# Performance work log

Measured on AMD Instinct MI355X. Metric: run time of the kernel, lower is better.

## Reference

```python
import jax, jax.numpy as jnp
import numpy as np

LN_EPS = 1e-5

def _layernorm(x, g, b):
    mu = jnp.mean(x, axis=-1, keepdims=True)
    var = jnp.mean(jnp.square(x - mu), axis=-1, keepdims=True)
    return (x - mu) * jax.lax.rsqrt(var + LN_EPS) * g + b

def setup_inputs() -> dict:
    key = jax.random.key(0)
    ks = jax.random.split(key, 8)
    B, T, C = 4, 2048, 1024
    s = 0.02
    return {
        "x": jax.random.normal(ks[0], (B, T, C), jnp.float32),
        "w_qkv": jax.random.normal(ks[1], (C, 3 * C), jnp.float32) * s,
        "b_qkv": jnp.zeros((3 * C,), jnp.float32),
        "w_out": jax.random.normal(ks[2], (C, C), jnp.float32) * s,
        "b_out": jnp.zeros((C,), jnp.float32),
        "w1": jax.random.normal(ks[3], (C, 4 * C), jnp.float32) * s,
        "b1": jnp.zeros((4 * C,), jnp.float32),
        "w2": jax.random.normal(ks[4], (4 * C, C), jnp.float32) * s,
        "b2": jnp.zeros((C,), jnp.float32),
        "g1": jnp.ones((C,), jnp.float32),
        "be1": jnp.zeros((C,), jnp.float32),
        "g2": jnp.ones((C,), jnp.float32),
        "be2": jnp.zeros((C,), jnp.float32),
        "n_head": 16,
    }

def reference(x, w_qkv, b_qkv, w_out, b_out, w1, b1, w2, b2, g1, be1, g2, be2, n_head):
    B, T, C = x.shape
    H = n_head
    D = C // H
    # --- causal self-attention ---
    qkv = x @ w_qkv + b_qkv                      # [B,T,3C]
    q, k, v = jnp.split(qkv, 3, axis=-1)
    q = q.reshape(B, T, H, D).transpose(0, 2, 1, 3)  # [B,H,T,D]
    k = k.reshape(B, T, H, D).transpose(0, 2, 1, 3)
    v = v.reshape(B, T, H, D).transpose(0, 2, 1, 3)
    attn = jnp.einsum("bhqd,bhkd->bhqk", q, k) * (1.0 / np.sqrt(D))
    causal = jnp.tril(jnp.ones((T, T), bool))
    attn = jnp.where(causal, attn, jnp.float32(-jnp.inf))
    attn = jax.nn.softmax(attn, axis=-1)
    y = jnp.einsum("bhqk,bhkd->bhqd", attn, v)
    y = y.transpose(0, 2, 1, 3).reshape(B, T, C)
    y = y @ w_out + b_out
    # post-norm residual (norm applied to sublayer output)
    x = x + _layernorm(y, g1, be1)
    # --- MLP ---
    h = jax.nn.gelu(x @ w1 + b1, approximate=False)
    h = h @ w2 + b2
    x = x + _layernorm(h, g2, be2)
    return x
```

## Files before the change

kernel.cpp:

```cpp
#include <hip/hip_runtime.h>
#include <hip/hip_bf16.h>

typedef unsigned short ushort_t;
using bf16x8 = __attribute__((ext_vector_type(8))) short;
using f32x4  = __attribute__((ext_vector_type(4))) float;

#define DEV __device__ __forceinline__

DEV unsigned short f2bf(float f) {
    unsigned int u = __builtin_bit_cast(unsigned int, f);
    u = (u + 0x7fffu + ((u >> 16) & 1u)) >> 16;
    return (unsigned short)u;
}

DEV int cvtpk_bf16(float lo, float hi) {
    int r;
    asm("v_cvt_pk_bf16_f32 %0, %1, %2" : "=v"(r) : "v"(lo), "v"(hi));
    return r;
}

DEV void gload16(const unsigned short* g, unsigned short* l) {
    __builtin_amdgcn_global_load_lds(
        (const __attribute__((address_space(1))) void*)g,
        (__attribute__((address_space(3))) void*)l, 16, 0, 0);
}

DEV float gelu_f(float v) {
    float u = v * (0.79788456f + 0.03567741f * v * v);
    float t = __builtin_amdgcn_exp2f(u * 2.88539008f);
    return v * t * __builtin_amdgcn_rcpf(t + 1.0f);
}

__global__ __launch_bounds__(256) void cvtbf_kernel(const float* __restrict__ in,
                                                    unsigned short* __restrict__ out) {
    int i = (blockIdx.x * 256 + threadIdx.x) * 4;
    float4 v = *(const float4*)&in[i];
    out[i + 0] = f2bf(v.x);
    out[i + 1] = f2bf(v.y);
    out[i + 2] = f2bf(v.z);
    out[i + 3] = f2bf(v.w);
}

__global__ __launch_bounds__(256) void transpose_cvt_kernel(const float* __restrict__ in,
                                                            unsigned short* __restrict__ out,
                                                            int R, int C) {
    __shared__ float t[32][33];
    int tx = threadIdx.x, ty = threadIdx.y;
    int c0 = blockIdx.x * 32, r0 = blockIdx.y * 32;
#pragma unroll
    for (int i = 0; i < 4; ++i)
        t[ty + i * 8][tx] = in[(size_t)(r0 + ty + i * 8) * C + c0 + tx];
    __syncthreads();
#pragma unroll
    for (int i = 0; i < 4; ++i)
        out[(size_t)(c0 + ty + i * 8) * R + r0 + tx] = f2bf(t[tx][ty + i * 8]);
}

__global__ __launch_bounds__(256) void vtrans_kernel(const unsigned short* __restrict__ qkvb,
                                                     unsigned short* __restrict__ vtg) {
    __shared__ unsigned short t[64 * 66];
    const int tid = threadIdx.x;
    const int t0 = blockIdx.x * 64;
    const int bh = blockIdx.y;
    const int b = bh >> 4, h = bh & 15;
    const unsigned short* src = qkvb + (size_t)(b * 2048 + t0) * 3072 + 2048 + h * 64;
#pragma unroll
    for (int c = 0; c < 2; ++c) {
        int cid = c * 256 + tid;
        int row = cid >> 3, cc = cid & 7;
        *(int4*)&t[row * 66 + cc * 8] = *(const int4*)&src[(size_t)row * 3072 + cc * 8];
    }
    __syncthreads();
    unsigned short* dst = vtg + (size_t)bh * 64 * 2048 + t0;
#pragma unroll
    for (int c = 0; c < 2; ++c) {
        int cid = c * 256 + tid;
        int d = cid >> 3, cc2 = cid & 7;
        bf16x8 v;
#pragma unroll
        for (int j = 0; j < 8; ++j) v[j] = (short)t[(cc2 * 8 + j) * 66 + d];
        *(bf16x8*)&dst[(size_t)d * 2048 + cc2 * 8] = v;
    }
}

template <int BM, int ACT, int OBF>
__global__ __launch_bounds__(512, 2) void gemm256_kernel(
    const unsigned short* __restrict__ A, const unsigned short* __restrict__ Bt,
    const float* __restrict__ bias, void* __restrict__ out,
    int N, int K, int gridNt) {
    constexpr int MF = BM / 32;
    constexpr int ALD = BM / 64;
    constexpr int NW = ALD / 2 + 2;
    constexpr int LB = (BM == 256) ? 8 : 7;
    __shared__ __align__(16) unsigned short lA[2][BM * 64];
    __shared__ __align__(16) unsigned short lB[2][256 * 64];
    const int tid = threadIdx.x;
    const int lane = tid & 63, wid = tid >> 6;
    const int g = lane >> 4, lr = lane & 15;
    const int wm = wid >> 2, wn = wid & 3;

    const int nwg = gridDim.x, cpx = nwg >> 3, bid = blockIdx.x;
    const int wkid = (bid & 7) * cpx + (bid >> 3);
    const int mt = wkid / gridNt, nt = wkid % gridNt;
    const int m0 = mt * BM, n0 = nt * 256;

    auto stageA = [&](int s, int kt, int bb) {
        int c = s * 512 + tid;
        int row = c & (BM - 1), kb = c >> LB;
        gload16(&A[(size_t)(m0 + row) * K + kt * 64 + kb * 8],
                &lA[bb][(size_t)(s * 512 + (tid & ~63)) * 8]);
    };
    auto stageB = [&](int s, int kt, int bb) {
        int c = s * 512 + tid;
        int row = c & 255, kb = c >> 8;
        gload16(&Bt[(size_t)(n0 + row) * K + kt * 64 + kb * 8],
                &lB[bb][(size_t)(s * 512 + (tid & ~63)) * 8]);
    };
    auto stageKh = [&](int half, int kt, int bb) {
        if constexpr (BM == 256) {
            stageA(half * 2 + 0, kt, bb);
            stageA(half * 2 + 1, kt, bb);
            stageB(half * 2 + 0, kt, bb);
            stageB(half * 2 + 1, kt, bb);
        } else {
            stageA(half, kt, bb);
            stageB(half * 2 + 0, kt, bb);
            stageB(half * 2 + 1, kt, bb);
        }
    };

    f32x4 acc[MF][4] = {};
    bf16x8 af[MF];
    bf16x8 bfr[4];

    const int nkt = K >> 6;
    stageKh(0, 0, 0);
    stageKh(1, 0, 0);

    for (int kt = 0; kt < nkt; ++kt) {
        const int b = kt & 1;
        const bool more = (kt + 1 < nkt);
#pragma unroll
        for (int ks = 0; ks < 2; ++ks) {
            if (ks == 1 && !more)
                asm volatile("s_waitcnt vmcnt(0)" ::: "memory");
            else if constexpr (BM == 256)
                asm volatile("s_waitcnt vmcnt(4)" ::: "memory");
            else
                asm volatile("s_waitcnt vmcnt(3)" ::: "memory");
            __builtin_amdgcn_s_barrier();
            asm volatile("" ::: "memory");
#pragma unroll
            for (int mf = 0; mf < MF; ++mf) {
                int c = (ks * 4 + g) * BM + wm * (BM / 2) + mf * 16 + lr;
                af[mf] = *(const bf16x8*)&lA[b][(size_t)c * 8];
            }
#pragma unroll
            for (int nf = 0; nf < 4; ++nf) {
                int c = (ks * 4 + g) * 256 + wn * 64 + nf * 16 + lr;
                bfr[nf] = *(const bf16x8*)&lB[b][(size_t)c * 8];
            }
            if (more) stageKh(ks, kt + 1, b ^ 1);
            __builtin_amdgcn_s_setprio(1);
#pragma unroll
            for (int mf = 0; mf < MF; ++mf)
#pragma unroll
                for (int nf = 0; nf < 4; ++nf)
                    acc[mf][nf] = __builtin_amdgcn_mfma_f32_16x16x32_bf16(
                        af[mf], bfr[nf], acc[mf][nf], 0, 0, 0);
            __builtin_amdgcn_s_setprio(0);
        }
    }

#pragma unroll
    for (int mf = 0; mf < MF; ++mf) {
#pragma unroll
        for (int nf = 0; nf < 4; ++nf) {
            int col = n0 + wn * 64 + nf * 16 + lr;
            float bv = bias[col];
#pragma unroll
            for (int r = 0; r < 4; ++r) {
                int row = m0 + wm * (BM / 2) + mf * 16 + g * 4 + r;
                float v = acc[mf][nf][r] + bv;
                if (ACT == 1) v = gelu_f(v);
                if (OBF)
                    ((unsigned short*)out)[(size_t)row * N + col] = f2bf(v);
                else
                    ((float*)out)[(size_t)row * N + col] = v;
            }
        }
    }
}

__global__ __launch_bounds__(256) void attn_kernel(const unsigned short* __restrict__ qkv,
                                                   const unsigned short* __restrict__ vtg,
                                                   unsigned short* __restrict__ y) {
    __shared__ unsigned short Kl[2][4096];
    __shared__ unsigned short Vl[2][4096];
    const int tid = threadIdx.x, lane = tid & 63, w = tid >> 6;
    const int g = lane >> 4, lr = lane & 15;
    const int p = blockIdx.x, h = blockIdx.y, b = blockIdx.z;
    const int bh = b * 16 + h;
    const size_t rs3 = 3072;
    const unsigned short* qbase = qkv + (size_t)b * 2048 * rs3 + h * 64;
    const unsigned short* kbase = qbase + 1024;
    const unsigned short* vbase = vtg + (size_t)bh * 64 * 2048;

    int ksoff[2], vsoff[2], ldoff[2];
#pragma unroll
    for (int c = 0; c < 2; ++c) {
        int row = w * 16 + c * 8 + (lane >> 3);
        int ccs = (lane & 7) ^ (row & 7) ^ (row >> 3);
        ksoff[c] = row * 3072 + ccs * 8;
        vsoff[c] = row * 2048 + ccs * 8;
        ldoff[c] = (w * 16 + c * 8) * 64;
    }

    const int idxP0 = 4 * (32 * (g & 1) + lr);
    const int idxP1 = idxP0 + 64;
    int idxA[4];
#pragma unroll
    for (int r = 0; r < 4; ++r) idxA[r] = 4 * (g * 20 + r);
    const bool ghigh = (g >> 1) != 0;
    const float qscale = 0.125f * 1.44269504089f;

    auto process = [&](int J) {
        const int q0w = J * 128 + w * 32;
        const int ktend = 2 * J + 2;
#pragma unroll
        for (int c = 0; c < 2; ++c) {
            gload16(&kbase[ksoff[c]], &Kl[0][ldoff[c]]);
            gload16(&vbase[vsoff[c]], &Vl[0][ldoff[c]]);
        }
        int qf[2][2][4];
#pragma unroll
        for (int sub = 0; sub < 2; ++sub)
#pragma unroll
            for (int f = 0; f < 2; ++f) {
                int4 v = *(const int4*)&qbase[(size_t)(q0w + sub * 16 + lr) * rs3 + f * 32 + g * 8];
                int vv[4] = {v.x, v.y, v.z, v.w};
#pragma unroll
                for (int i = 0; i < 4; ++i) {
                    unsigned int u = (unsigned int)vv[i];
                    float lo = __builtin_bit_cast(float, u << 16) * qscale;
                    float hi = __builtin_bit_cast(float, u & 0xffff0000u) * qscale;
                    qf[sub][f][i] = cvtpk_bf16(lo, hi);
                }
            }

        f32x4 O[2][4] = {};
        float m_[2] = {-3.0e38f, -3.0e38f}, l_[2] = {0.f, 0.f};

        int buf = 0;
        for (int kt = 0; kt < ktend; ++kt) {
            asm volatile("s_waitcnt vmcnt(0)" ::: "memory");
            __builtin_amdgcn_s_barrier();
            asm volatile("" ::: "memory");
            if (kt + 1 < ktend) {
#pragma unroll
                for (int c = 0; c < 2; ++c) {
                    gload16(&kbase[(size_t)(kt + 1) * 64 * 3072 + ksoff[c]], &Kl[buf ^ 1][ldoff[c]]);
                    gload16(&vbase[vsoff[c] + (kt + 1) * 64], &Vl[buf ^ 1][ldoff[c]]);
                }
            }
            const unsigned short* Kc = Kl[buf];
            const unsigned short* Vc = Vl[buf];

            const bool act0 = (kt * 64) <= (q0w + 15);
            const bool act1 = (kt * 64) <= (q0w + 31);

            f32x4 s0[4], s1[4];
#pragma unroll
            for (int st = 0; st < 4; ++st) {
                int rbase = (st * 16 + lr) * 64;
                int sw = (lr & 7) ^ (st * 2 + (lr >> 3));
                bf16x8 kf0 = *(const bf16x8*)&Kc[rbase + ((g ^ sw) * 8)];
                bf16x8 kf1 = *(const bf16x8*)&Kc[rbase + (((4 + g) ^ sw) * 8)];
                if (act0) {
                    f32x4 a = {};
                    a = __builtin_amdgcn_mfma_f32_16x16x32_bf16(kf0, *(const bf16x8*)&qf[0][0], a, 0, 0, 0);
                    a = __builtin_amdgcn_mfma_f32_16x16x32_bf16(kf1, *(const bf16x8*)&qf[0][1], a, 0, 0, 0);
                    s0[st] = a;
                }
                if (act1) {
                    f32x4 a = {};
                    a = __builtin_amdgcn_mfma_f32_16x16x32_bf16(kf0, *(const bf16x8*)&qf[1][0], a, 0, 0, 0);
                    a = __builtin_amdgcn_mfma_f32_16x16x32_bf16(kf1, *(const bf16x8*)&qf[1][1], a, 0, 0, 0);
                    s1[st] = a;
                }
            }

            int wt0[2][4], wt1[2][4];
#pragma unroll
            for (int sub = 0; sub < 2; ++sub) {
                if (sub == 0 && !act0) continue;
                if (sub == 1 && !act1) continue;
                f32x4* s = (sub == 0) ? s0 : s1;
                const int qmin = q0w + sub * 16;
                if (kt * 64 + 63 > qmin) {
                    int qv = qmin + lr;
#pragma unroll
                    for (int st = 0; st < 4; ++st) {
                        int keyb = kt * 64 + st * 16 + g * 4;
#pragma unroll
                        for (int r = 0; r < 4; ++r)
                            if (keyb + r > qv) s[st][r] = -3.0e38f;
                    }
                }
                float mx = fmaxf(fmaxf(s[0][0], s[0][1]), fmaxf(s[0][2], s[0][3]));
#pragma unroll
                for (int st = 1; st < 4; ++st)
                    mx = fmaxf(mx, fmaxf(fmaxf(s[st][0], s[st][1]), fmaxf(s[st][2], s[st][3])));
                mx = fmaxf(mx, __shfl_xor(mx, 16));
                mx = fmaxf(mx, __shfl_xor(mx, 32));
                float mold = m_[sub];
                float mnew = fmaxf(mold, mx);
                float alpha = __builtin_amdgcn_exp2f(mold - mnew);
                m_[sub] = mnew;
                float rs = 0.f;
#pragma unroll
                for (int st = 0; st < 4; ++st)
#pragma unroll
                    for (int r = 0; r < 4; ++r) {
                        float pp = __builtin_amdgcn_exp2f(s[st][r] - mnew);
                        s[st][r] = pp;
                        rs += pp;
                    }
                rs += __shfl_xor(rs, 16);
                rs += __shfl_xor(rs, 32);
                l_[sub] = l_[sub] * alpha + rs;
                int av = __builtin_bit_cast(int, alpha);
                f32x4* Os = O[sub];
#pragma unroll
                for (int r = 0; r < 4; ++r) {
                    float ar = __builtin_bit_cast(float, __builtin_amdgcn_ds_bpermute(idxA[r], av));
#pragma unroll
                    for (int dt = 0; dt < 4; ++dt) Os[dt][r] *= ar;
                }
                int ws_[4][2];
#pragma unroll
                for (int st = 0; st < 4; ++st) {
                    ws_[st][0] = cvtpk_bf16(s[st][0], s[st][1]);
                    ws_[st][1] = cvtpk_bf16(s[st][2], s[st][3]);
                }
                int(*wt)[4] = (sub == 0) ? wt0 : wt1;
#pragma unroll
                for (int ks = 0; ks < 2; ++ks)
#pragma unroll
                    for (int hp = 0; hp < 4; ++hp) {
                        int idx = (hp < 2) ? idxP0 : idxP1;
                        int v0 = __builtin_amdgcn_ds_bpermute(idx, ws_[2 * ks][hp & 1]);
                        int v1 = __builtin_amdgcn_ds_bpermute(idx, ws_[2 * ks + 1][hp & 1]);
                        wt[ks][hp] = ghigh ? v1 : v0;
                    }
            }

#pragma unroll
            for (int ks = 0; ks < 2; ++ks) {
                bf16x8 pa0 = *(const bf16x8*)&wt0[ks][0];
                bf16x8 pa1 = *(const bf16x8*)&wt1[ks][0];
#pragma unroll
                for (int dt = 0; dt < 4; ++dt) {
                    int d = dt * 16 + lr;
                    int xv = (ks * 4 + g) ^ (lr & 7) ^ (dt * 2 + (lr >> 3));
                    bf16x8 vf = *(const bf16x8*)&Vc[d * 64 + xv * 8];
                    if (act0) O[0][dt] = __builtin_amdgcn_mfma_f32_16x16x32_bf16(pa0, vf, O[0][dt], 0, 0, 0);
                    if (act1) O[1][dt] = __builtin_amdgcn_mfma_f32_16x16x32_bf16(pa1, vf, O[1][dt], 0, 0, 0);
                }
            }
            buf ^= 1;
        }

#pragma unroll
        for (int sub = 0; sub < 2; ++sub) {
            int lv = __builtin_bit_cast(int, l_[sub]);
#pragma unroll
            for (int r = 0; r < 4; ++r) {
                float lval = __builtin_bit_cast(float, __builtin_amdgcn_ds_bpermute(idxA[r], lv));
                float inv = __builtin_amdgcn_rcpf(lval);
                int q = q0w + sub * 16 + g * 4 + r;
#pragma unroll
                for (int dt = 0; dt < 4; ++dt)
                    y[(size_t)(b * 2048 + q) * 1024 + h * 64 + dt * 16 + lr] =
                        f2bf(O[sub][dt][r] * inv);
            }
        }
    };

    process(15 - p);
    __syncthreads();
    process(p);
}

template <int WRITE_BF>
__global__ __launch_bounds__(256) void ln_kernel(const float* __restrict__ base,
                                                 const float* __restrict__ delta,
                                                 const float* __restrict__ gw,
                                                 const float* __restrict__ bw,
                                                 float* __restrict__ outf,
                                                 unsigned short* __restrict__ outb) {
    const int row = blockIdx.x;
    const int tid = threadIdx.x;
    const float* d = delta + (size_t)row * 1024;
    const float* bs = base + (size_t)row * 1024;
    float4 x = *(const float4*)&d[tid * 4];
    float s = x.x + x.y + x.z + x.w;
    float s2 = x.x * x.x + x.y * x.y + x.z * x.z + x.w * x.w;
#pragma unroll
    for (int off = 1; off < 64; off <<= 1) {
        s += __shfl_xor(s, off);
        s2 += __shfl_xor(s2, off);
    }
    __shared__ float red[8];
    if ((tid & 63) == 0) {
        red[tid >> 6] = s;
        red[4 + (tid >> 6)] = s2;
    }
    __syncthreads();
    s = red[0] + red[1] + red[2] + red[3];
    s2 = red[4] + red[5] + red[6] + red[7];
    float mu = s * (1.f / 1024.f);
    float var = s2 * (1.f / 1024.f) - mu * mu;
    float rsig = rsqrtf(var + 1e-5f);
    float4 bb = *(const float4*)&bs[tid * 4];
    float4 gv = *(const float4*)&gw[tid * 4];
    float4 bv = *(const float4*)&bw[tid * 4];
    float4 o;
    o.x = bb.x + (x.x - mu) * rsig * gv.x + bv.x;
    o.y = bb.y + (x.y - mu) * rsig * gv.y + bv.y;
    o.z = bb.z + (x.z - mu) * rsig * gv.z + bv.z;
    o.w = bb.w + (x.w - mu) * rsig * gv.w + bv.w;
    *(float4*)&outf[(size_t)row * 1024 + tid * 4] = o;
    if (WRITE_BF) {
        unsigned short* ob = outb + (size_t)row * 1024 + tid * 4;
        ob[0] = f2bf(o.x);
        ob[1] = f2bf(o.y);
        ob[2] = f2bf(o.z);
        ob[3] = f2bf(o.w);
    }
}

extern "C" void kernel_launch(void* const* d_in, const int* in_sizes, int n_in,
                              void* d_out, int out_size, void* d_ws, size_t ws_size,
                              hipStream_t stream) {
    const float* x = (const float*)d_in[0];
    const float* w_qkv = (const float*)d_in[1];
    const float* b_qkv = (const float*)d_in[2];
    const float* w_out = (const float*)d_in[3];
    const float* b_out = (const float*)d_in[4];
    const float* w1 = (const float*)d_in[5];
    const float* b1 = (const float*)d_in[6];
    const float* w2 = (const float*)d_in[7];
    const float* b2 = (const float*)d_in[8];
    const float* g1 = (const float*)d_in[9];
    const float* be1 = (const float*)d_in[10];
    const float* g2 = (const float*)d_in[11];
    const float* be2 = (const float*)d_in[12];

    const size_t MB = 1ull << 20;
    if (ws_size < 184 * MB) return;
    char* ws = (char*)d_ws;
    unsigned short* xb    = (unsigned short*)(ws + 0);
    unsigned short* vtg   = (unsigned short*)(ws + 0);
    unsigned short* wqkvt = (unsigned short*)(ws + 16 * MB);
    unsigned short* qkvb  = (unsigned short*)(ws + 22 * MB);
    unsigned short* hb    = (unsigned short*)(ws + 0);
    unsigned short* woutt = (unsigned short*)(ws + 70 * MB);
    unsigned short* yb    = (unsigned short*)(ws + 72 * MB);
    float*          attnp = (float*)(ws + 88 * MB);
    float*          ff    = (float*)(ws + 88 * MB);
    float*          x2f   = (float*)(ws + 120 * MB);
    unsigned short* x2b   = (unsigned short*)(ws + 152 * MB);
    unsigned short* w1t   = (unsigned short*)(ws + 168 * MB);
    unsigned short* w2t   = (unsigned short*)(ws + 176 * MB);

    cvtbf_kernel<<<8192, 256, 0, stream>>>(x, xb);
    transpose_cvt_kernel<<<dim3(96, 32), dim3(32, 8), 0, stream>>>(w_qkv, wqkvt, 1024, 3072);
    transpose_cvt_kernel<<<dim3(32, 32), dim3(32, 8), 0, stream>>>(w_out, woutt, 1024, 1024);
    transpose_cvt_kernel<<<dim3(128, 32), dim3(32, 8), 0, stream>>>(w1, w1t, 1024, 4096);
    transpose_cvt_kernel<<<dim3(32, 128), dim3(32, 8), 0, stream>>>(w2, w2t, 4096, 1024);
    gemm256_kernel<256, 0, 1><<<384, 512, 0, stream>>>(xb, wqkvt, b_qkv, qkvb, 3072, 1024, 12);
    vtrans_kernel<<<dim3(32, 64), 256, 0, stream>>>(qkvb, vtg);
    attn_kernel<<<dim3(8, 16, 4), 256, 0, stream>>>(qkvb, vtg, yb);
    gemm256_kernel<128, 0, 0><<<256, 512, 0, stream>>>(yb, woutt, b_out, attnp, 1024, 1024, 4);
    ln_kernel<1><<<8192, 256, 0, stream>>>(x, attnp, g1, be1, x2f, x2b);
    gemm256_kernel<256, 1, 1><<<512, 512, 0, stream>>>(x2b, w1t, b1, hb, 4096, 1024, 16);
    gemm256_kernel<128, 0, 0><<<256, 512, 0, stream>>>(hb, w2t, b2, ff, 1024, 4096, 4);
    ln_kernel<0><<<8192, 256, 0, stream>>>(x2f, ff, g2, be2, (float*)d_out, nullptr);
}
```

Before: 511.6 us.

## Restructure GEMM main loops into finer-grained phases with prefetch before barriers

Splits the templated GEMM into separate 256-row and 128-row kernels. The 256-row kernel now runs four phases per K tile, each handling half of the M fragments, and interleaves the next tile's global-to-LDS loads across those phases. Both kernels prefetch before the loop, add sched_barriers and lgkmcnt waits around the MFMA blocks, and reorder vmcnt waits so loads overlap the matrix math. This also cuts the live A-fragment registers, in exchange for twice as many barriers per tile.

```diff
diff --git a/kernel.cpp b/kernel.cpp
--- a/kernel.cpp
+++ b/kernel.cpp
@@ -83,16 +83,12 @@
     }
 }
 
-template <int BM, int ACT, int OBF>
+template <int ACT, int OBF>
 __global__ __launch_bounds__(512, 2) void gemm256_kernel(
     const unsigned short* __restrict__ A, const unsigned short* __restrict__ Bt,
     const float* __restrict__ bias, void* __restrict__ out,
     int N, int K, int gridNt) {
-    constexpr int MF = BM / 32;
-    constexpr int ALD = BM / 64;
-    constexpr int NW = ALD / 2 + 2;
-    constexpr int LB = (BM == 256) ? 8 : 7;
-    __shared__ __align__(16) unsigned short lA[2][BM * 64];
+    __shared__ __align__(16) unsigned short lA[2][256 * 64];
     __shared__ __align__(16) unsigned short lB[2][256 * 64];
     const int tid = threadIdx.x;
     const int lane = tid & 63, wid = tid >> 6;
@@ -102,11 +98,11 @@
     const int nwg = gridDim.x, cpx = nwg >> 3, bid = blockIdx.x;
     const int wkid = (bid & 7) * cpx + (bid >> 3);
     const int mt = wkid / gridNt, nt = wkid % gridNt;
-    const int m0 = mt * BM, n0 = nt * 256;
+    const int m0 = mt * 256, n0 = nt * 256;
 
     auto stageA = [&](int s, int kt, int bb) {
         int c = s * 512 + tid;
-        int row = c & (BM - 1), kb = c >> LB;
+        int row = c & 255, kb = c >> 8;
         gload16(&A[(size_t)(m0 + row) * K + kt * 64 + kb * 8],
                 &lA[bb][(size_t)(s * 512 + (tid & ~63)) * 8]);
     };
@@ -116,71 +112,176 @@
         gload16(&Bt[(size_t)(n0 + row) * K + kt * 64 + kb * 8],
                 &lB[bb][(size_t)(s * 512 + (tid & ~63)) * 8]);
     };
-    auto stageKh = [&](int half, int kt, int bb) {
-        if constexpr (BM == 256) {
-            stageA(half * 2 + 0, kt, bb);
-            stageA(half * 2 + 1, kt, bb);
-            stageB(half * 2 + 0, kt, bb);
-            stageB(half * 2 + 1, kt, bb);
-        } else {
-            stageA(half, kt, bb);
-            stageB(half * 2 + 0, kt, bb);
-            stageB(half * 2 + 1, kt, bb);
-        }
-    };
-
-    f32x4 acc[MF][4] = {};
-    bf16x8 af[MF];
+
+    f32x4 acc[8][4] = {};
     bf16x8 bfr[4];
-
     const int nkt = K >> 6;
-    stageKh(0, 0, 0);
-    stageKh(1, 0, 0);
+
+    stageA(0, 0, 0); stageA(1, 0, 0); stageB(0, 0, 0); stageB(1, 0, 0);
+    stageA(2, 0, 0); stageA(3, 0, 0); stageB(2, 0, 0); stageB(3, 0, 0);
+    asm volatile("s_waitcnt vmcnt(4)" ::: "memory");
+    __builtin_amdgcn_s_barrier();
+    asm volatile("" ::: "memory");
 
     for (int kt = 0; kt < nkt; ++kt) {
-        const int b = kt & 1;
+        const int buf = kt & 1;
         const bool more = (kt + 1 < nkt);
 #pragma unroll
-        for (int ks = 0; ks < 2; ++ks) {
-            if (ks == 1 && !more)
-                asm volatile("s_waitcnt vmcnt(0)" ::: "memory");
-            else if constexpr (BM == 256)
-                asm volatile("s_waitcnt vmcnt(4)" ::: "memory");
-            else
-                asm volatile("s_waitcnt vmcnt(3)" ::: "memory");
+        for (int p = 0; p < 4; ++p) {
+            const int ks = p >> 1, mh = p & 1;
+            bf16x8 af[4];
+#pragma unroll
+            for (int mf2 = 0; mf2 < 4; ++mf2) {
+                int c = (ks * 4 + g) * 256 + wm * 128 + (mh * 4 + mf2) * 16 + lr;
+                af[mf2] = *(const bf16x8*)&lA[buf][(size_t)c * 8];
+            }
+            if (mh == 0) {
+#pragma unroll
+                for (int nf = 0; nf < 4; ++nf) {
+                    int c = (ks * 4 + g) * 256 + wn * 64 + nf * 16 + lr;
+                    bfr[nf] = *(const bf16x8*)&lB[buf][(size_t)c * 8];
+                }
+            }
+            if (more) {
+                if (p == 0)      { stageA(0, kt + 1, buf ^ 1); stageA(1, kt + 1, buf ^ 1); }
+                else if (p == 1) { stageB(0, kt + 1, buf ^ 1); stageB(1, kt + 1, buf ^ 1); }
+                else if (p == 2) { stageA(2, kt + 1, buf ^ 1); stageA(3, kt + 1, buf ^ 1); }
+                else             { stageB(2, kt + 1, buf ^ 1); stageB(3, kt + 1, buf ^ 1); }
+            }
+            __builtin_amdgcn_s_barrier();
+            asm volatile("s_waitcnt lgkmcnt(0)" ::: "memory");
+            __builtin_amdgcn_sched_barrier(0);
+            __builtin_amdgcn_s_setprio(1);
+#pragma unroll
+            for (int mf2 = 0; mf2 < 4; ++mf2)
+#pragma unroll
+                for (int nf = 0; nf < 4; ++nf)
+                    acc[mh * 4 + mf2][nf] = __builtin_amdgcn_mfma_f32_16x16x32_bf16(
+                        af[mf2], bfr[nf], acc[mh * 4 + mf2][nf], 0, 0, 0);
+            __builtin_amdgcn_s_setprio(0);
+            __builtin_amdgcn_sched_barrier(0);
+            if (p == 1) {
+                if (more) asm volatile("s_waitcnt vmcnt(4)" ::: "memory");
+                else      asm volatile("s_waitcnt vmcnt(0)" ::: "memory");
+            } else if (p == 3) {
+                if (more) asm volatile("s_waitcnt vmcnt(4)" ::: "memory");
+            }
             __builtin_amdgcn_s_barrier();
             asm volatile("" ::: "memory");
-#pragma unroll
-            for (int mf = 0; mf < MF; ++mf) {
-                int c = (ks * 4 + g) * BM + wm * (BM / 2) + mf * 16 + lr;
-                af[mf] = *(const bf16x8*)&lA[b][(size_t)c * 8];
+        }
+    }
+
+#pragma unroll
+    for (int mf = 0; mf < 8; ++mf) {
+#pragma unroll
+        for (int nf = 0; nf < 4; ++nf) {
+            int col = n0 + wn * 64 + nf * 16 + lr;
+            float bv = bias[col];
+#pragma unroll
+            for (int r = 0; r < 4; ++r) {
+                int row = m0 + wm * 128 + mf * 16 + g * 4 + r;
+                float v = acc[mf][nf][r] + bv;
+                if (ACT == 1) v = gelu_f(v);
+                if (OBF)
+                    ((unsigned short*)out)[(size_t)row * N + col] = f2bf(v);
+                else
+                    ((float*)out)[(size_t)row * N + col] = v;
+            }
+        }
+    }
+}
+
+template <int ACT, int OBF>
+__global__ __launch_bounds__(512, 2) void gemm128_kernel(
+    const unsigned short* __restrict__ A, const unsigned short* __restrict__ Bt,
+    const float* __restrict__ bias, void* __restrict__ out,
+    int N, int K, int gridNt) {
+    __shared__ __align__(16) unsigned short lA[2][128 * 64];
+    __shared__ __align__(16) unsigned short lB[2][256 * 64];
+    const int tid = threadIdx.x;
+    const int lane = tid & 63, wid = tid >> 6;
+    const int g = lane >> 4, lr = lane & 15;
+    const int wm = wid >> 2, wn = wid & 3;
+
+    const int nwg = gridDim.x, cpx = nwg >> 3, bid = blockIdx.x;
+    const int wkid = (bid & 7) * cpx + (bid >> 3);
+    const int mt = wkid / gridNt, nt = wkid % gridNt;
+    const int m0 = mt * 128, n0 = nt * 256;
+
+    auto stageA = [&](int s, int kt, int bb) {
+        int c = s * 512 + tid;
+        int row = c & 127, kb = c >> 7;
+        gload16(&A[(size_t)(m0 + row) * K + kt * 64 + kb * 8],
+                &lA[bb][(size_t)(s * 512 + (tid & ~63)) * 8]);
+    };
+    auto stageB = [&](int s, int kt, int bb) {
+        int c = s * 512 + tid;
+        int row = c & 255, kb = c >> 8;
+        gload16(&Bt[(size_t)(n0 + row) * K + kt * 64 + kb * 8],
+                &lB[bb][(size_t)(s * 512 + (tid & ~63)) * 8]);
+    };
+
+    f32x4 acc[4][4] = {};
+    const int nkt = K >> 6;
+
+    stageA(0, 0, 0); stageB(0, 0, 0); stageB(1, 0, 0);
+    stageA(1, 0, 0); stageB(2, 0, 0); stageB(3, 0, 0);
+    asm volatile("s_waitcnt vmcnt(3)" ::: "memory");
+    __builtin_amdgcn_s_barrier();
+    asm volatile("" ::: "memory");
+
+    for (int kt = 0; kt < nkt; ++kt) {
+        const int buf = kt & 1;
+        const bool more = (kt + 1 < nkt);
+#pragma unroll
+        for (int ks = 0; ks < 2; ++ks) {
+            bf16x8 af[4], bfr[4];
+#pragma unroll
+            for (int mf = 0; mf < 4; ++mf) {
+                int c = (ks * 4 + g) * 128 + wm * 64 + mf * 16 + lr;
+                af[mf] = *(const bf16x8*)&lA[buf][(size_t)c * 8];
             }
 #pragma unroll
             for (int nf = 0; nf < 4; ++nf) {
                 int c = (ks * 4 + g) * 256 + wn * 64 + nf * 16 + lr;
-                bfr[nf] = *(const bf16x8*)&lB[b][(size_t)c * 8];
-            }
-            if (more) stageKh(ks, kt + 1, b ^ 1);
+                bfr[nf] = *(const bf16x8*)&lB[buf][(size_t)c * 8];
+            }
+            if (more) {
+                if (ks == 0) { stageA(0, kt + 1, buf ^ 1); stageB(0, kt + 1, buf ^ 1); stageB(1, kt + 1, buf ^ 1); }
+                else         { stageA(1, kt + 1, buf ^ 1); stageB(2, kt + 1, buf ^ 1); stageB(3, kt + 1, buf ^ 1); }
+            }
+            __builtin_amdgcn_s_barrier();
+            asm volatile("s_waitcnt lgkmcnt(0)" ::: "memory");
+            __builtin_amdgcn_sched_barrier(0);
             __builtin_amdgcn_s_setprio(1);
 #pragma unroll
-            for (int mf = 0; mf < MF; ++mf)
+            for (int mf = 0; mf < 4; ++mf)
 #pragma unroll
                 for (int nf = 0; nf < 4; ++nf)
                     acc[mf][nf] = __builtin_amdgcn_mfma_f32_16x16x32_bf16(
                         af[mf], bfr[nf], acc[mf][nf], 0, 0, 0);
             __builtin_amdgcn_s_setprio(0);
-        }
-    }
-
-#pragma unroll
-    for (int mf = 0; mf < MF; ++mf) {
+            __builtin_amdgcn_sched_barrier(0);
+            if (ks == 0) {
+                if (more) asm volatile("s_waitcnt vmcnt(3)" ::: "memory");
+                else      asm volatile("s_waitcnt vmcnt(0)" ::: "memory");
+            } else {
+                if (more) asm volatile("s_waitcnt vmcnt(3)" ::: "memory");
+            }
+            __builtin_amdgcn_s_barrier();
+            asm volatile("" ::: "memory");
+        }
+    }
+
+#pragma unroll
+    for (int mf = 0; mf < 4; ++mf) {
 #pragma unroll
         for (int nf = 0; nf < 4; ++nf) {
             int col = n0 + wn * 64 + nf * 16 + lr;
             float bv = bias[col];
 #pragma unroll
             for (int r = 0; r < 4; ++r) {
-                int row = m0 + wm * (BM / 2) + mf * 16 + g * 4 + r;
+                int row = m0 + wm * 64 + mf * 16 + g * 4 + r;
                 float v = acc[mf][nf][r] + bv;
                 if (ACT == 1) v = gelu_f(v);
                 if (OBF)
@@ -479,12 +580,12 @@
     transpose_cvt_kernel<<<dim3(32, 32), dim3(32, 8), 0, stream>>>(w_out, woutt, 1024, 1024);
     transpose_cvt_kernel<<<dim3(128, 32), dim3(32, 8), 0, stream>>>(w1, w1t, 1024, 4096);
     transpose_cvt_kernel<<<dim3(32, 128), dim3(32, 8), 0, stream>>>(w2, w2t, 4096, 1024);
-    gemm256_kernel<256, 0, 1><<<384, 512, 0, stream>>>(xb, wqkvt, b_qkv, qkvb, 3072, 1024, 12);
+    gemm256_kernel<0, 1><<<384, 512, 0, stream>>>(xb, wqkvt, b_qkv, qkvb, 3072, 1024, 12);
     vtrans_kernel<<<dim3(32, 64), 256, 0, stream>>>(qkvb, vtg);
     attn_kernel<<<dim3(8, 16, 4), 256, 0, stream>>>(qkvb, vtg, yb);
-    gemm256_kernel<128, 0, 0><<<256, 512, 0, stream>>>(yb, woutt, b_out, attnp, 1024, 1024, 4);
+    gemm128_kernel<0, 0><<<256, 512, 0, stream>>>(yb, woutt, b_out, attnp, 1024, 1024, 4);
     ln_kernel<1><<<8192, 256, 0, stream>>>(x, attnp, g1, be1, x2f, x2b);
-    gemm256_kernel<256, 1, 1><<<512, 512, 0, stream>>>(x2b, w1t, b1, hb, 4096, 1024, 16);
-    gemm256_kernel<128, 0, 0><<<256, 512, 0, stream>>>(hb, w2t, b2, ff, 1024, 4096, 4);
+    gemm256_kernel<1, 1><<<512, 512, 0, stream>>>(x2b, w1t, b1, hb, 4096, 1024, 16);
+    gemm128_kernel<0, 0><<<256, 512, 0, stream>>>(hb, w2t, b2, ff, 1024, 4096, 4);
     ln_kernel<0><<<8192, 256, 0, stream>>>(x2f, ff, g2, be2, (float*)d_out, nullptr);
 }
```

Result: no change. 505.4 us (-1.2%).
